# Kernel tuning notes

Measured on AMD Instinct MI355X. Metric: run time of the kernel, lower is better.

Reference implementation:

```python
import jax, jax.numpy as jnp
import numpy as np

HEADS = 8
DIM = 64      # dim
DH = 64       # dim_head
DK = 24       # dim_k (== dim_head_k * heads, required by reshape in forward)
DHK = 3       # dim_head_k (also conv groups)


def setup_inputs() -> dict:
    key = jax.random.key(0)
    ks = jax.random.split(key, 10)
    b, h, w = 4, 128, 128
    return {
        "x_in": jax.random.normal(ks[0], (b, h, w, DIM), jnp.float32),
        "illu_fea_trans": jax.random.normal(ks[1], (b, h, w, DIM), jnp.float32),
        "illu_map_trans": jax.random.normal(ks[2], (b, h, w, DK), jnp.float32),
        # Linear weights stored as [in, out] (torch stores [out, in]; math y = x @ W_in_out)
        "Wq": jax.random.normal(ks[3], (DIM, HEADS * DH), jnp.float32) * 0.05,
        "Wk": jax.random.normal(ks[4], (DK, HEADS * DHK), jnp.float32) * 0.05,
        "Wv": jax.random.normal(ks[5], (DIM, HEADS * DH), jnp.float32) * 0.05,
        "rescale": jnp.ones((HEADS, 1, 1), jnp.float32),
        "Wp": jax.random.normal(ks[6], (HEADS * DHK, DK), jnp.float32) * 0.05,
        "bp": jax.random.normal(ks[7], (DK,), jnp.float32) * 0.05,
        # grouped conv weights, OIHW: [out=24, in/groups=8, 3, 3]
        "conv1_w": jax.random.normal(ks[8], (DK, DK // DHK, 3, 3), jnp.float32) * 0.05,
        "conv2_w": jax.random.normal(ks[9], (DK, DK // DHK, 3, 3), jnp.float32) * 0.05,
    }


def _gconv(x_nchw, w_oihw):
    return jax.lax.conv_general_dilated(
        x_nchw, w_oihw, window_strides=(1, 1), padding='SAME',
        feature_group_count=DHK,
        dimension_numbers=('NCHW', 'OIHW', 'NCHW'))


def reference(x_in, illu_fea_trans, illu_map_trans, Wq, Wk, Wv, rescale, Wp, bp, conv1_w, conv2_w):
    b, h, w, c = x_in.shape
    n = h * w
    # projections
    q = (x_in.reshape(b, n, c) @ Wq).reshape(b, n, HEADS, DH)
    k_inp = illu_map_trans.reshape(b, n, DK) @ Wk            # [b, n, heads*dhk]
    v = (illu_fea_trans.reshape(b, n, c) @ Wv).reshape(b, n, HEADS, DH)
    kh = k_inp.reshape(b, n, HEADS, DHK)
    q = q / (DIM ** 0.5)  # note: scaled by sqrt(dim), not sqrt(dim_head)
    # channel-wise cross-attention: attn over channel dims, contracting tokens n
    attn = jnp.einsum('bnhk,bnhd->bhkd', kh, q) * rescale[None]  # [b, heads, dhk, dh]
    attn = jax.nn.softmax(attn, axis=-1)
    out = jnp.einsum('bhkd,bnhd->bnkh', attn, v)             # [b, n, dhk, heads]
    out = out.reshape(b, n, DHK * HEADS) @ Wp + bp           # proj
    out = out.reshape(b, h, w, DK)
    # positional branch: two grouped 3x3 convs with exact GELU on k_inp
    kx = k_inp.reshape(b, h, w, DK).transpose(0, 3, 1, 2)    # NCHW
    y = _gconv(kx, conv1_w)
    y = jax.nn.gelu(y, approximate=False)
    y = _gconv(y, conv2_w)
    return out + y.transpose(0, 2, 3, 1)
```

## Files before the change

### kernel.cpp

```cpp
#include <hip/hip_runtime.h>
#include <math.h>

#define HEADS 8
#define DIM   64
#define DK    24
#define DHK   3
#define BB    4
#define HH    128
#define WW    128
#define NN    (HH*WW)
#define QSCALE 0.125f

__global__ __launch_bounds__(256) void s_reduce(
    const float* __restrict__ imap,
    const float* __restrict__ x,
    float* __restrict__ Sp)
{
    __shared__ float part[4*1536];
    const int tid = threadIdx.x;
    const int blk = blockIdx.x;
    const int b = blk >> 7, chunk = blk & 127;
    const int w = tid >> 6, lane = tid & 63;
    const int cq = lane & 15;
    const int ig = lane >> 4;

    const long tok0 = (long)b * NN + chunk * 128 + w * 32;
    const float* xp = x    + tok0 * 64 + cq * 4;
    const float* mp = imap + tok0 * 24 + ig * 6;

    float acc[6][4];
    #pragma unroll
    for (int r = 0; r < 6; ++r)
        #pragma unroll
        for (int q = 0; q < 4; ++q) acc[r][q] = 0.f;

    for (int t = 0; t < 32; ++t) {
        float4 xv = *(const float4*)(xp + t * 64);
        float2 m0 = *(const float2*)(mp + t * 24);
        float2 m1 = *(const float2*)(mp + t * 24 + 2);
        float2 m2 = *(const float2*)(mp + t * 24 + 4);
        float mm[6] = {m0.x, m0.y, m1.x, m1.y, m2.x, m2.y};
        #pragma unroll
        for (int r = 0; r < 6; ++r) {
            acc[r][0] += mm[r] * xv.x;
            acc[r][1] += mm[r] * xv.y;
            acc[r][2] += mm[r] * xv.z;
            acc[r][3] += mm[r] * xv.w;
        }
    }

    float* pp = part + w * 1536;
    #pragma unroll
    for (int r = 0; r < 6; ++r) {
        float4 v = {acc[r][0], acc[r][1], acc[r][2], acc[r][3]};
        *(float4*)(pp + (ig * 6 + r) * 64 + cq * 4) = v;
    }
    __syncthreads();

    for (int e = tid; e < 1536; e += 256) {
        float s = part[e] + part[1536 + e] + part[3072 + e] + part[4608 + e];
        atomicAdd(&Sp[b * 1536 + e], s);
    }
}

__global__ __launch_bounds__(256) void attn_p(
    const float* __restrict__ Sp,
    const float* __restrict__ Wk,
    const float* __restrict__ Wq,
    const float* __restrict__ Wv,
    const float* __restrict__ rescale,
    const float* __restrict__ Wp,
    float* __restrict__ Pt)
{
    __shared__ float Sp_l[1536];
    __shared__ float S_l[1536];
    __shared__ float att[1536];
    __shared__ float M_l[1536];

    const int b = blockIdx.x, tid = threadIdx.x;

    for (int i = tid; i < 1536; i += 256) Sp_l[i] = Sp[b * 1536 + i];
    __syncthreads();

    for (int q = tid; q < 1536; q += 256) {
        int c = q & 63, j = q >> 6;
        float s = 0.f;
        #pragma unroll
        for (int i = 0; i < 24; ++i) s += Wk[i * 24 + j] * Sp_l[i * 64 + c];
        S_l[q] = s;
    }
    __syncthreads();

    for (int q = tid; q < 1536; q += 256) {
        int d = q & 63, ch = q >> 6;
        int h = ch / 3;
        const float* wq = Wq + h * 64 + d;
        const float* sr = S_l + ch * 64;
        float s = 0.f;
        for (int cc = 0; cc < 64; ++cc) s += sr[cc] * wq[cc * 512];
        att[q] = s * QSCALE * rescale[h];
    }
    __syncthreads();

    if (tid < 24) {
        float* row = att + tid * 64;
        float mx = row[0];
        for (int d = 1; d < 64; ++d) mx = fmaxf(mx, row[d]);
        float sum = 0.f;
        for (int d = 0; d < 64; ++d) { float e = expf(row[d] - mx); row[d] = e; sum += e; }
        float inv = 1.f / sum;
        for (int d = 0; d < 64; ++d) row[d] *= inv;
    }
    __syncthreads();

    for (int q = tid; q < 1536; q += 256) {
        int c = q & 63, ch = q >> 6;
        int h = ch / 3;
        const float* wv = Wv + c * 512 + h * 64;
        const float* ar = att + ch * 64;
        float s = 0.f;
        for (int d = 0; d < 64; ++d) s += ar[d] * wv[d];
        M_l[ch * 64 + c] = s;
    }
    __syncthreads();

    for (int q = tid; q < 1536; q += 256) {
        int c = q & 63, jo = q >> 6;
        float s = 0.f;
        #pragma unroll
        for (int k = 0; k < 3; ++k)
            #pragma unroll
            for (int h = 0; h < 8; ++h)
                s += M_l[(h * 3 + k) * 64 + c] * Wp[(k * 8 + h) * 24 + jo];
        Pt[b * 1536 + q] = s;
    }
}

__global__ __launch_bounds__(256) void k_proj(
    const float* __restrict__ imap, const float* __restrict__ Wk,
    float* __restrict__ k_inp)
{
    __shared__ float kbuf[256 * 25];
    const int tid = threadIdx.x;
    const long base = (long)blockIdx.x * 256;

    const float4* m4 = (const float4*)(imap + (base + tid) * 24);
    float m[24];
    #pragma unroll
    for (int i = 0; i < 6; ++i) {
        float4 v = m4[i];
        m[4*i+0]=v.x; m[4*i+1]=v.y; m[4*i+2]=v.z; m[4*i+3]=v.w;
    }
    float kv[24];
    #pragma unroll
    for (int j = 0; j < 24; ++j) kv[j] = 0.f;
    for (int i = 0; i < 24; ++i) {
        float mi = m[i];
        #pragma unroll
        for (int j = 0; j < 24; ++j) kv[j] += mi * Wk[i * 24 + j];
    }
    #pragma unroll
    for (int j = 0; j < 24; ++j) kbuf[tid * 25 + j] = kv[j];
    __syncthreads();

    for (int e = tid; e < 6144; e += 256)
        k_inp[base * 24 + e] = kbuf[(e / 24) * 25 + (e % 24)];
}

template <bool GELU, bool ACCUM>
__device__ __forceinline__ void gconv_body(
    const float* __restrict__ in, const float* __restrict__ cw,
    float* __restrict__ outp)
{
    const int tid = threadIdx.x;
    const int o = tid % 24, jj = tid / 24;
    const int blk = blockIdx.x;
    const int b = blk >> 8, ti = (blk >> 4) & 15, tj = blk & 15;
    const int i0 = ti * 8, j0 = tj * 8;
    const int g = o >> 3;

    float wr[8][9];
    {
        const float4* wp = (const float4*)(cw + o * 72);
        #pragma unroll
        for (int t = 0; t < 18; ++t) ((float4*)wr)[t] = wp[t];
    }

    const int gj0 = j0 + jj - 1;
    const bool cok0 = gj0 >= 0;
    const bool cok2 = (j0 + jj + 1) < WW;
    const float* basep = in + (long)b * NN * 24 + g * 8;

    float win[3][3][8];

    #define LOADROW(GI, SLOT)                                                 \
    {                                                                         \
        const int gi_ = (GI);                                                 \
        const bool rok_ = (gi_ >= 0) & (gi_ < HH);                            \
        const float* rp_ = basep + ((long)gi_ * WW + gj0) * 24;               \
        float4 z_ = {0.f,0.f,0.f,0.f};                                        \
        float4 a0_=z_, a1_=z_, b0_=z_, b1_=z_, c0_=z_, c1_=z_;                \
        if (rok_ & cok0) { a0_ = *(const float4*)(rp_);                       \
                           a1_ = *(const float4*)(rp_ + 4); }                 \
        if (rok_)        { b0_ = *(const float4*)(rp_ + 24);                  \
                           b1_ = *(const float4*)(rp_ + 28); }                \
        if (rok_ & cok2) { c0_ = *(const float4*)(rp_ + 48);                  \
                           c1_ = *(const float4*)(rp_ + 52); }                \
        *(float4*)&win[SLOT][0][0] = a0_; *(float4*)&win[SLOT][0][4] = a1_;   \
        *(float4*)&win[SLOT][1][0] = b0_; *(float4*)&win[SLOT][1][4] = b1_;   \
        *(float4*)&win[SLOT][2][0] = c0_; *(float4*)&win[SLOT][2][4] = c1_;   \
    }

    LOADROW(i0 - 1, 0)
    LOADROW(i0,     1)

    #pragma unroll
    for (int ii = 0; ii < 8; ++ii) {
        LOADROW(i0 + ii + 1, (ii + 2) % 3)
        float s = 0.f;
        #pragma unroll
        for (int di = 0; di < 3; ++di) {
            const int slot = (ii + di) % 3;
            #pragma unroll
            for (int dj = 0; dj < 3; ++dj)
                #pragma unroll
                for (int ic = 0; ic < 8; ++ic)
                    s += win[slot][dj][ic] * wr[ic][di * 3 + dj];
        }
        if (GELU) s = 0.5f * s * (1.f + erff(s * 0.70710678f));
        const long idx = ((long)((b * HH + i0 + ii) * WW + j0)) * 24 + tid;
        if (ACCUM) outp[idx] = outp[idx] + s;
        else       outp[idx] = s;
    }
    #undef LOADROW
}

__global__ __launch_bounds__(192, 2) void conv1_gelu(
    const float* __restrict__ kin, const float* __restrict__ cw,
    float* __restrict__ y1)
{
    gconv_body<true, false>(kin, cw, y1);
}

__global__ __launch_bounds__(192, 2) void conv2_add(
    const float* __restrict__ y1, const float* __restrict__ cw,
    float* __restrict__ outp)
{
    gconv_body<false, true>(y1, cw, outp);
}

__global__ __launch_bounds__(256) void proj_out(
    const float* __restrict__ fea,
    const float* __restrict__ Pt,
    const float* __restrict__ bp,
    float* __restrict__ outp)
{
    __shared__ float Pt_l[1536];
    __shared__ float obuf[256 * 25];

    const int tid = threadIdx.x;
    const int blk = blockIdx.x;
    const int b = blk >> 6, tile = blk & 63;
    const long pix0 = (long)b * NN + tile * 256;

    for (int e = tid; e < 1536; e += 256) Pt_l[e] = Pt[b * 1536 + e];
    __syncthreads();

    const int lane = tid & 63, og = tid >> 6;

    float acc[4][6];
    #pragma unroll
    for (int k = 0; k < 4; ++k)
        #pragma unroll
        for (int r = 0; r < 6; ++r) acc[k][r] = 0.f;

    const float* f0 = fea + (pix0 + lane) * 64;

    for (int cq = 0; cq < 16; ++cq) {
        float4 f[4];
        #pragma unroll
        for (int k = 0; k < 4; ++k)
            f[k] = *(const float4*)(f0 + 4096 * k + cq * 4);
        #pragma unroll
        for (int r = 0; r < 6; ++r) {
            float4 p = *(const float4*)(Pt_l + (og * 6 + r) * 64 + cq * 4);
            #pragma unroll
            for (int k = 0; k < 4; ++k) {
                acc[k][r] += f[k].x * p.x;
                acc[k][r] += f[k].y * p.y;
                acc[k][r] += f[k].z * p.z;
                acc[k][r] += f[k].w * p.w;
            }
        }
    }

    float bias[6];
    #pragma unroll
    for (int r = 0; r < 6; ++r) bias[r] = bp[og * 6 + r];

    #pragma unroll
    for (int k = 0; k < 4; ++k)
        #pragma unroll
        for (int r = 0; r < 6; ++r)
            obuf[(lane + 64 * k) * 25 + og * 6 + r] = acc[k][r] + bias[r];
    __syncthreads();

    for (int e = tid; e < 6144; e += 256)
        outp[pix0 * 24 + e] = obuf[(e / 24) * 25 + (e % 24)];
}

extern "C" void kernel_launch(void* const* d_in, const int* in_sizes, int n_in,
                              void* d_out, int out_size, void* d_ws, size_t ws_size,
                              hipStream_t stream) {
    const float* x_in    = (const float*)d_in[0];
    const float* fea     = (const float*)d_in[1];
    const float* imap    = (const float*)d_in[2];
    const float* Wq      = (const float*)d_in[3];
    const float* Wk      = (const float*)d_in[4];
    const float* Wv      = (const float*)d_in[5];
    const float* rescale = (const float*)d_in[6];
    const float* Wp      = (const float*)d_in[7];
    const float* bp      = (const float*)d_in[8];
    const float* c1w     = (const float*)d_in[9];
    const float* c2w     = (const float*)d_in[10];
    float* out = (float*)d_out;

    float* ws    = (float*)d_ws;
    float* k_inp = ws;
    float* y1    = ws + 1572864;
    float* Sp    = ws + 3145728;
    float* Pt    = ws + 3151872;

    hipMemsetAsync(Sp, 0, 6144 * sizeof(float), stream);
    s_reduce<<<512, 256, 0, stream>>>(imap, x_in, Sp);
    attn_p<<<4, 256, 0, stream>>>(Sp, Wk, Wq, Wv, rescale, Wp, Pt);
    k_proj<<<256, 256, 0, stream>>>(imap, Wk, k_inp);
    conv1_gelu<<<BB * 256, 192, 0, stream>>>(k_inp, c1w, y1);
    proj_out<<<256, 256, 0, stream>>>(fea, Pt, bp, out);
    conv2_add<<<BB * 256, 192, 0, stream>>>(y1, c2w, out);
}
```

Before: 182.6 us.

## Fuse k-projection into S reduction and projection into conv2, drop atomics

The k_inp projection moves into the S reduction kernel, reusing the imap tokens each block already reads, and per-block partials are written to a buffer that a small kernel then sums in place of global atomics and the memset. The output projection (fea·Pt + bias) is folded into the second conv kernel, so the output is written once and not read back and rewritten. This removes two launches and the extra out-buffer traffic. The cost is an extra reduction kernel and more per-thread work in conv2, where the fea reads are strided per thread and may coalesce worse.

```diff
diff --git a/kernel.cpp b/kernel.cpp
--- a/kernel.cpp
+++ b/kernel.cpp
@@ -11,12 +11,14 @@
 #define NN    (HH*WW)
 #define QSCALE 0.125f
 
-__global__ __launch_bounds__(256) void s_reduce(
+__global__ __launch_bounds__(256) void s_reduce_kproj(
     const float* __restrict__ imap,
     const float* __restrict__ x,
-    float* __restrict__ Sp)
-{
-    __shared__ float part[4*1536];
+    const float* __restrict__ Wk,
+    float* __restrict__ k_inp,
+    float* __restrict__ Sp_part)
+{
+    __shared__ float lds[4*1536];
     const int tid = threadIdx.x;
     const int blk = blockIdx.x;
     const int b = blk >> 7, chunk = blk & 127;
@@ -24,7 +26,8 @@
     const int cq = lane & 15;
     const int ig = lane >> 4;
 
-    const long tok0 = (long)b * NN + chunk * 128 + w * 32;
+    const long tokB = (long)b * NN + chunk * 128;
+    const long tok0 = tokB + w * 32;
     const float* xp = x    + tok0 * 64 + cq * 4;
     const float* mp = imap + tok0 * 24 + ig * 6;
 
@@ -49,7 +52,7 @@
         }
     }
 
-    float* pp = part + w * 1536;
+    float* pp = lds + w * 1536;
     #pragma unroll
     for (int r = 0; r < 6; ++r) {
         float4 v = {acc[r][0], acc[r][1], acc[r][2], acc[r][3]};
@@ -57,10 +60,52 @@
     }
     __syncthreads();
 
-    for (int e = tid; e < 1536; e += 256) {
-        float s = part[e] + part[1536 + e] + part[3072 + e] + part[4608 + e];
-        atomicAdd(&Sp[b * 1536 + e], s);
-    }
+    for (int e = tid; e < 1536; e += 256)
+        Sp_part[(long)blk * 1536 + e] =
+            lds[e] + lds[1536 + e] + lds[3072 + e] + lds[4608 + e];
+
+    float kv[24];
+    if (tid < 128) {
+        const float4* m4 = (const float4*)(imap + (tokB + tid) * 24);
+        float m[24];
+        #pragma unroll
+        for (int i = 0; i < 6; ++i) {
+            float4 v = m4[i];
+            m[4*i+0]=v.x; m[4*i+1]=v.y; m[4*i+2]=v.z; m[4*i+3]=v.w;
+        }
+        #pragma unroll
+        for (int j = 0; j < 24; ++j) kv[j] = 0.f;
+        for (int i = 0; i < 24; ++i) {
+            float mi = m[i];
+            #pragma unroll
+            for (int j = 0; j < 24; ++j) kv[j] += mi * Wk[i * 24 + j];
+        }
+    }
+    __syncthreads();
+    if (tid < 128) {
+        #pragma unroll
+        for (int j = 0; j < 24; ++j) lds[tid * 25 + j] = kv[j];
+    }
+    __syncthreads();
+    for (int e = tid; e < 128 * 24; e += 256)
+        k_inp[tokB * 24 + e] = lds[(e / 24) * 25 + (e % 24)];
+}
+
+__global__ __launch_bounds__(256) void sp_reduce(
+    const float* __restrict__ Sp_part, float* __restrict__ Sp)
+{
+    const int blk = blockIdx.x;
+    const int b = blk / 6, eb = blk % 6;
+    const int e = eb * 256 + threadIdx.x;
+    const float* p = Sp_part + (long)b * 128 * 1536 + e;
+    float s0 = 0.f, s1 = 0.f, s2 = 0.f, s3 = 0.f;
+    for (int c = 0; c < 128; c += 4) {
+        s0 += p[(long)(c + 0) * 1536];
+        s1 += p[(long)(c + 1) * 1536];
+        s2 += p[(long)(c + 2) * 1536];
+        s3 += p[(long)(c + 3) * 1536];
+    }
+    Sp[b * 1536 + e] = (s0 + s1) + (s2 + s3);
 }
 
 __global__ __launch_bounds__(256) void attn_p(
@@ -136,68 +181,29 @@
     }
 }
 
-__global__ __launch_bounds__(256) void k_proj(
-    const float* __restrict__ imap, const float* __restrict__ Wk,
-    float* __restrict__ k_inp)
-{
-    __shared__ float kbuf[256 * 25];
-    const int tid = threadIdx.x;
-    const long base = (long)blockIdx.x * 256;
-
-    const float4* m4 = (const float4*)(imap + (base + tid) * 24);
-    float m[24];
-    #pragma unroll
-    for (int i = 0; i < 6; ++i) {
-        float4 v = m4[i];
-        m[4*i+0]=v.x; m[4*i+1]=v.y; m[4*i+2]=v.z; m[4*i+3]=v.w;
-    }
-    float kv[24];
-    #pragma unroll
-    for (int j = 0; j < 24; ++j) kv[j] = 0.f;
-    for (int i = 0; i < 24; ++i) {
-        float mi = m[i];
-        #pragma unroll
-        for (int j = 0; j < 24; ++j) kv[j] += mi * Wk[i * 24 + j];
-    }
-    #pragma unroll
-    for (int j = 0; j < 24; ++j) kbuf[tid * 25 + j] = kv[j];
-    __syncthreads();
-
-    for (int e = tid; e < 6144; e += 256)
-        k_inp[base * 24 + e] = kbuf[(e / 24) * 25 + (e % 24)];
-}
-
-template <bool GELU, bool ACCUM>
-__device__ __forceinline__ void gconv_body(
-    const float* __restrict__ in, const float* __restrict__ cw,
-    float* __restrict__ outp)
-{
-    const int tid = threadIdx.x;
-    const int o = tid % 24, jj = tid / 24;
-    const int blk = blockIdx.x;
-    const int b = blk >> 8, ti = (blk >> 4) & 15, tj = blk & 15;
-    const int i0 = ti * 8, j0 = tj * 8;
-    const int g = o >> 3;
-
-    float wr[8][9];
-    {
-        const float4* wp = (const float4*)(cw + o * 72);
-        #pragma unroll
-        for (int t = 0; t < 18; ++t) ((float4*)wr)[t] = wp[t];
-    }
-
-    const int gj0 = j0 + jj - 1;
-    const bool cok0 = gj0 >= 0;
+#define CONV_PROLOG(CWPTR)                                                    \
+    const int tid = threadIdx.x;                                              \
+    const int o = tid % 24, jj = tid / 24;                                    \
+    const int blk = blockIdx.x;                                               \
+    const int b = blk >> 8, ti = (blk >> 4) & 15, tj = blk & 15;              \
+    const int i0 = ti * 8, j0 = tj * 8;                                       \
+    const int g = o >> 3;                                                     \
+    float wr[8][9];                                                           \
+    {                                                                         \
+        const float4* wp = (const float4*)((CWPTR) + o * 72);                 \
+        _Pragma("unroll")                                                     \
+        for (int t = 0; t < 18; ++t) ((float4*)wr)[t] = wp[t];                \
+    }                                                                         \
+    const int gj0 = j0 + jj - 1;                                              \
+    const bool cok0 = gj0 >= 0;                                               \
     const bool cok2 = (j0 + jj + 1) < WW;
-    const float* basep = in + (long)b * NN * 24 + g * 8;
-
-    float win[3][3][8];
-
-    #define LOADROW(GI, SLOT)                                                 \
+
+#define LOADROW(IN, GI, SLOT)                                                 \
     {                                                                         \
         const int gi_ = (GI);                                                 \
         const bool rok_ = (gi_ >= 0) & (gi_ < HH);                            \
-        const float* rp_ = basep + ((long)gi_ * WW + gj0) * 24;               \
+        const float* rp_ = (IN) + (long)b * NN * 24 + g * 8                   \
+                         + ((long)gi_ * WW + gj0) * 24;                       \
         float4 z_ = {0.f,0.f,0.f,0.f};                                        \
         float4 a0_=z_, a1_=z_, b0_=z_, b1_=z_, c0_=z_, c1_=z_;                \
         if (rok_ & cok0) { a0_ = *(const float4*)(rp_);                       \
@@ -211,12 +217,17 @@
         *(float4*)&win[SLOT][2][0] = c0_; *(float4*)&win[SLOT][2][4] = c1_;   \
     }
 
-    LOADROW(i0 - 1, 0)
-    LOADROW(i0,     1)
-
+__global__ __launch_bounds__(192, 2) void conv1_gelu(
+    const float* __restrict__ kin, const float* __restrict__ cw,
+    float* __restrict__ y1)
+{
+    CONV_PROLOG(cw)
+    float win[3][3][8];
+    LOADROW(kin, i0 - 1, 0)
+    LOADROW(kin, i0,     1)
     #pragma unroll
     for (int ii = 0; ii < 8; ++ii) {
-        LOADROW(i0 + ii + 1, (ii + 2) % 3)
+        LOADROW(kin, i0 + ii + 1, (ii + 2) % 3)
         float s = 0.f;
         #pragma unroll
         for (int di = 0; di < 3; ++di) {
@@ -227,86 +238,53 @@
                 for (int ic = 0; ic < 8; ++ic)
                     s += win[slot][dj][ic] * wr[ic][di * 3 + dj];
         }
-        if (GELU) s = 0.5f * s * (1.f + erff(s * 0.70710678f));
-        const long idx = ((long)((b * HH + i0 + ii) * WW + j0)) * 24 + tid;
-        if (ACCUM) outp[idx] = outp[idx] + s;
-        else       outp[idx] = s;
-    }
-    #undef LOADROW
-}
-
-__global__ __launch_bounds__(192, 2) void conv1_gelu(
-    const float* __restrict__ kin, const float* __restrict__ cw,
-    float* __restrict__ y1)
-{
-    gconv_body<true, false>(kin, cw, y1);
-}
-
-__global__ __launch_bounds__(192, 2) void conv2_add(
-    const float* __restrict__ y1, const float* __restrict__ cw,
-    float* __restrict__ outp)
-{
-    gconv_body<false, true>(y1, cw, outp);
-}
-
-__global__ __launch_bounds__(256) void proj_out(
-    const float* __restrict__ fea,
-    const float* __restrict__ Pt,
-    const float* __restrict__ bp,
-    float* __restrict__ outp)
-{
-    __shared__ float Pt_l[1536];
-    __shared__ float obuf[256 * 25];
-
-    const int tid = threadIdx.x;
-    const int blk = blockIdx.x;
-    const int b = blk >> 6, tile = blk & 63;
-    const long pix0 = (long)b * NN + tile * 256;
-
-    for (int e = tid; e < 1536; e += 256) Pt_l[e] = Pt[b * 1536 + e];
-    __syncthreads();
-
-    const int lane = tid & 63, og = tid >> 6;
-
-    float acc[4][6];
+        s = 0.5f * s * (1.f + erff(s * 0.70710678f));
+        y1[((long)((b * HH + i0 + ii) * WW + j0)) * 24 + tid] = s;
+    }
+}
+
+__global__ __launch_bounds__(192, 2) void conv2_proj(
+    const float* __restrict__ y1, const float* __restrict__ fea,
+    const float* __restrict__ cw2, const float* __restrict__ Pt,
+    const float* __restrict__ bp, float* __restrict__ outp)
+{
+    CONV_PROLOG(cw2)
+
+    float acc[8];
+    {
+        const float bo = bp[o];
+        #pragma unroll
+        for (int ii = 0; ii < 8; ++ii) acc[ii] = bo;
+        const float* PtRow = Pt + b * 1536 + o * 64;
+        const float* feaB = fea + (((long)(b * HH + i0)) * WW + (j0 + jj)) * 64;
+        for (int cq = 0; cq < 16; ++cq) {
+            float4 p = *(const float4*)(PtRow + cq * 4);
+            #pragma unroll
+            for (int ii = 0; ii < 8; ++ii) {
+                float4 f = *(const float4*)(feaB + (long)ii * WW * 64 + cq * 4);
+                acc[ii] += f.x * p.x + f.y * p.y + f.z * p.z + f.w * p.w;
+            }
+        }
+    }
+
+    float win[3][3][8];
+    LOADROW(y1, i0 - 1, 0)
+    LOADROW(y1, i0,     1)
     #pragma unroll
-    for (int k = 0; k < 4; ++k)
-        #pragma unroll
-        for (int r = 0; r < 6; ++r) acc[k][r] = 0.f;
-
-    const float* f0 = fea + (pix0 + lane) * 64;
-
-    for (int cq = 0; cq < 16; ++cq) {
-        float4 f[4];
-        #pragma unroll
-        for (int k = 0; k < 4; ++k)
-            f[k] = *(const float4*)(f0 + 4096 * k + cq * 4);
-        #pragma unroll
-        for (int r = 0; r < 6; ++r) {
-            float4 p = *(const float4*)(Pt_l + (og * 6 + r) * 64 + cq * 4);
-            #pragma unroll
-            for (int k = 0; k < 4; ++k) {
-                acc[k][r] += f[k].x * p.x;
-                acc[k][r] += f[k].y * p.y;
-                acc[k][r] += f[k].z * p.z;
-                acc[k][r] += f[k].w * p.w;
-            }
-        }
-    }
-
-    float bias[6];
-    #pragma unroll
-    for (int r = 0; r < 6; ++r) bias[r] = bp[og * 6 + r];
-
-    #pragma unroll
-    for (int k = 0; k < 4; ++k)
-        #pragma unroll
-        for (int r = 0; r < 6; ++r)
-            obuf[(lane + 64 * k) * 25 + og * 6 + r] = acc[k][r] + bias[r];
-    __syncthreads();
-
-    for (int e = tid; e < 6144; e += 256)
-        outp[pix0 * 24 + e] = obuf[(e / 24) * 25 + (e % 24)];
+    for (int ii = 0; ii < 8; ++ii) {
+        LOADROW(y1, i0 + ii + 1, (ii + 2) % 3)
+        float s = 0.f;
+        #pragma unroll
+        for (int di = 0; di < 3; ++di) {
+            const int slot = (ii + di) % 3;
+            #pragma unroll
+            for (int dj = 0; dj < 3; ++dj)
+                #pragma unroll
+                for (int ic = 0; ic < 8; ++ic)
+                    s += win[slot][dj][ic] * wr[ic][di * 3 + dj];
+        }
+        outp[((long)((b * HH + i0 + ii) * WW + j0)) * 24 + tid] = acc[ii] + s;
+    }
 }
 
 extern "C" void kernel_launch(void* const* d_in, const int* in_sizes, int n_in,
@@ -325,17 +303,16 @@
     const float* c2w     = (const float*)d_in[10];
     float* out = (float*)d_out;
 
-    float* ws    = (float*)d_ws;
-    float* k_inp = ws;
-    float* y1    = ws + 1572864;
-    float* Sp    = ws + 3145728;
-    float* Pt    = ws + 3151872;
-
-    hipMemsetAsync(Sp, 0, 6144 * sizeof(float), stream);
-    s_reduce<<<512, 256, 0, stream>>>(imap, x_in, Sp);
+    float* ws      = (float*)d_ws;
+    float* k_inp   = ws;
+    float* y1      = ws + 1572864;
+    float* Sp_part = ws + 3145728;
+    float* Sp      = ws + 3932160;
+    float* Pt      = ws + 3938304;
+
+    s_reduce_kproj<<<512, 256, 0, stream>>>(imap, x_in, Wk, k_inp, Sp_part);
+    sp_reduce<<<24, 256, 0, stream>>>(Sp_part, Sp);
     attn_p<<<4, 256, 0, stream>>>(Sp, Wk, Wq, Wv, rescale, Wp, Pt);
-    k_proj<<<256, 256, 0, stream>>>(imap, Wk, k_inp);
     conv1_gelu<<<BB * 256, 192, 0, stream>>>(k_inp, c1w, y1);
-    proj_out<<<256, 256, 0, stream>>>(fea, Pt, bp, out);
-    conv2_add<<<BB * 256, 192, 0, stream>>>(y1, c2w, out);
-}
+    conv2_proj<<<BB * 256, 192, 0, stream>>>(y1, fea, c2w, Pt, bp, out);
+}
```

Result: faster. 178.8 us (-2.1%).
